# Optimization experiments

Hardware: AMD Instinct MI355X
Metric: run time of the kernel (lower is better)

Reference implementation:

```python
import jax, jax.numpy as jnp
import numpy as np


def setup_inputs() -> dict:
    key = jax.random.key(0)
    k1, k2, k3, k4 = jax.random.split(key, 4)
    B, S, I, H, O = 32, 4096, 64, 512, 64
    x = jax.random.normal(k1, (B, S, I), dtype=jnp.float32)
    b = jax.random.normal(k2, (I, H), dtype=jnp.float32)
    A = jax.random.uniform(k3, (H,), dtype=jnp.float32)  # stable diagonal decay in [0,1)
    c = jax.random.normal(k4, (H, O), dtype=jnp.float32)
    return {"x": x, "b": b, "A": A, "c": c}


def reference(x, b, A, c):
    # Diagonal-transition linear RNN: h_t = x_t @ b + h_{t-1} * A ; y_t = h_t @ c
    B, S, I = x.shape
    H = A.shape[0]
    xb = jnp.einsum('bsi,ih->sbh', x, b)  # precompute input projection, scan-major layout

    def step(h, xb_t):
        h = xb_t + h * A
        return h, h

    h0 = jnp.zeros((B, H), dtype=x.dtype)
    _, hs = jax.lax.scan(step, h0, xb)          # hs: [S, B, H]
    ys = jnp.einsum('sbh,ho->bso', hs, c)       # [B, S, O]
    # torch concat along dim=1 of per-step [B,O] outputs -> [B, S*O], then unsqueeze(-1)
    out = ys.reshape(B, S * ys.shape[-1])[:, :, None]
    return out
```

## Files before the change

kernel.cpp:

```cpp
#include <hip/hip_runtime.h>
#include <hip/hip_bf16.h>

constexpr int Bc = 32, Sc = 4096, Ic = 64, Hc = 512, Oc = 64;
constexpr int Lc = 128;
constexpr int NCc = Sc / Lc;
constexpr int HSUB = 128;
constexpr int NSUB = Hc / HSUB;

typedef __attribute__((ext_vector_type(8))) short short8;
typedef __attribute__((ext_vector_type(4))) short short4v;
typedef __attribute__((ext_vector_type(4))) float float4v;
typedef __attribute__((ext_vector_type(2))) unsigned uint2v;

__device__ __forceinline__ short f2bf(float f) {
    unsigned u = __builtin_bit_cast(unsigned, f);
    u += 0x7FFFu + ((u >> 16) & 1u);
    return (short)(u >> 16);
}
__device__ __forceinline__ float bf2f(short s) {
    unsigned u = ((unsigned)(unsigned short)s) << 16;
    return __builtin_bit_cast(float, u);
}

__device__ __forceinline__ int swz(int row, int rowBytes, int byteInRow) {
    return row * rowBytes + (byteInRow ^ ((row & 7) << 4));
}

__global__ void prep_kernel(const float* __restrict__ bw, const float* __restrict__ cw,
                            short* __restrict__ bT, short* __restrict__ cT) {
    int gid = blockIdx.x * 256 + threadIdx.x;
    if (gid < Ic * Hc) {
        int i = gid / Hc, h = gid % Hc;
        bT[h * Ic + i] = f2bf(bw[gid]);
    } else {
        int idx = gid - Ic * Hc;
        int h = idx / Oc, o = idx % Oc;
        cT[o * Hc + h] = f2bf(cw[idx]);
    }
}

__global__ void carry_kernel(const float* __restrict__ Adiag, const float* __restrict__ last,
                             float* __restrict__ carryIn) {
    int gid = blockIdx.x * 256 + threadIdx.x;
    int b = gid >> 9, h = gid & (Hc - 1);
    float a = Adiag[h];
    float aL = (a > 0.f) ? exp2f((float)Lc * log2f(a)) : 0.f;
    float run = 0.f;
    for (int k = 0; k < NCc; k++) {
        size_t idx = ((size_t)b * NCc + k) * Hc + h;
        carryIn[idx] = run;
        run = last[idx] + aL * run;
    }
}

template <int WRITE_Y>
__global__ __launch_bounds__(256, 2) void chunk_kernel(
    const float* __restrict__ x, const short* __restrict__ bT,
    const short* __restrict__ cT, const float* __restrict__ Adiag,
    const float* __restrict__ carryIn, float* __restrict__ lastOut,
    float* __restrict__ out) {
    __shared__ char Xs[128 * 128];
    __shared__ char bTs[128 * 128];
    __shared__ char cTs[64 * 256];
    __shared__ char xbh[128 * 256];

    const int tid = threadIdx.x;
    const int chunk = blockIdx.x, b = blockIdx.y;
    const int t0 = chunk * Lc;
    const int l = tid & 63;
    const int tg = (tid >> 6) * 32;

    const float4v* xg = (const float4v*)(x + ((size_t)b * Sc + t0) * Ic);
#pragma unroll
    for (int rr = 0; rr < 8; rr++) {
        int idx = rr * 256 + tid;
        float4v v = xg[idx];
        int row = idx >> 4, c4 = idx & 15;
        short4v sv;
        sv[0] = f2bf(v[0]); sv[1] = f2bf(v[1]); sv[2] = f2bf(v[2]); sv[3] = f2bf(v[3]);
        *(short4v*)(Xs + swz(row, 128, c4 * 8)) = sv;
    }

    float4v yacc[2][4];
    if (WRITE_Y) {
#pragma unroll
        for (int i = 0; i < 2; i++)
#pragma unroll
            for (int j = 0; j < 4; j++) yacc[i][j] = (float4v)0.f;
    }

    for (int hsu = 0; hsu < NSUB; hsu++) {
        __syncthreads();

        const uint2v* bg = (const uint2v*)(bT + hsu * HSUB * Ic);
#pragma unroll
        for (int rr = 0; rr < 8; rr++) {
            int idx = rr * 256 + tid;
            int row = idx >> 4, c8 = idx & 15;
            uint2v vv = bg[idx];
            *(uint2v*)(bTs + swz(row, 128, c8 * 8)) = vv;
        }
        if (WRITE_Y) {
            const uint2v* cg = (const uint2v*)cT;
#pragma unroll
            for (int rr = 0; rr < 8; rr++) {
                int idx = rr * 256 + tid;
                int row = idx >> 5, c8 = idx & 31;
                uint2v vv = cg[row * 128 + hsu * 32 + c8];
                *(uint2v*)(cTs + swz(row, 256, c8 * 8)) = vv;
            }
        }
        __syncthreads();

        short8 afr[2][2];
#pragma unroll
        for (int ti = 0; ti < 2; ti++)
#pragma unroll
            for (int ks = 0; ks < 2; ks++) {
                int row = tg + ti * 16 + (l & 15);
                int byt = ks * 64 + ((l >> 4) * 16);
                afr[ti][ks] = *(const short8*)(Xs + swz(row, 128, byt));
            }
#pragma unroll
        for (int hj = 0; hj < 8; hj++) {
            short8 bfr[2];
#pragma unroll
            for (int ks = 0; ks < 2; ks++) {
                int row = hj * 16 + (l & 15);
                int byt = ks * 64 + ((l >> 4) * 16);
                bfr[ks] = *(const short8*)(bTs + swz(row, 128, byt));
            }
#pragma unroll
            for (int ti = 0; ti < 2; ti++) {
                float4v acc = (float4v)0.f;
                acc = __builtin_amdgcn_mfma_f32_16x16x32_bf16(afr[ti][0], bfr[0], acc, 0, 0, 0);
                acc = __builtin_amdgcn_mfma_f32_16x16x32_bf16(afr[ti][1], bfr[1], acc, 0, 0, 0);
#pragma unroll
                for (int r = 0; r < 4; r++) {
                    int trow = tg + ti * 16 + (l >> 4) * 4 + r;
                    int hcol = hj * 16 + (l & 15);
                    *(short*)(xbh + swz(trow, 256, hcol * 2)) = f2bf(acc[r]);
                }
            }
        }
        __syncthreads();

        if (tid < HSUB) {
            int h = hsu * HSUB + tid;
            float a = Adiag[h];
            float hstate = WRITE_Y ? carryIn[((size_t)b * NCc + chunk) * Hc + h] : 0.f;
#pragma unroll 4
            for (int t = 0; t < Lc; t++) {
                int off = swz(t, 256, tid * 2);
                float v = bf2f(*(short*)(xbh + off));
                hstate = fmaf(hstate, a, v);
                if (WRITE_Y) *(short*)(xbh + off) = f2bf(hstate);
            }
            if (!WRITE_Y) lastOut[((size_t)b * NCc + chunk) * Hc + h] = hstate;
        }
        __syncthreads();

        if (WRITE_Y) {
#pragma unroll
            for (int ks = 0; ks < 4; ks++) {
                short8 a2[2];
#pragma unroll
                for (int ti = 0; ti < 2; ti++) {
                    int row = tg + ti * 16 + (l & 15);
                    int byt = ks * 64 + ((l >> 4) * 16);
                    a2[ti] = *(const short8*)(xbh + swz(row, 256, byt));
                }
#pragma unroll
                for (int oj = 0; oj < 4; oj++) {
                    int row = oj * 16 + (l & 15);
                    int byt = ks * 64 + ((l >> 4) * 16);
                    short8 b2 = *(const short8*)(cTs + swz(row, 256, byt));
#pragma unroll
                    for (int ti = 0; ti < 2; ti++)
                        yacc[ti][oj] = __builtin_amdgcn_mfma_f32_16x16x32_bf16(a2[ti], b2, yacc[ti][oj], 0, 0, 0);
                }
            }
        }
    }

    if (WRITE_Y) {
        float* og = out + ((size_t)b * Sc + t0) * Oc;
#pragma unroll
        for (int ti = 0; ti < 2; ti++)
#pragma unroll
            for (int oj = 0; oj < 4; oj++)
#pragma unroll
                for (int r = 0; r < 4; r++) {
                    int t = tg + ti * 16 + (l >> 4) * 4 + r;
                    int o = oj * 16 + (l & 15);
                    og[t * Oc + o] = yacc[ti][oj][r];
                }
    }
}

extern "C" void kernel_launch(void* const* d_in, const int* in_sizes, int n_in,
                              void* d_out, int out_size, void* d_ws, size_t ws_size,
                              hipStream_t stream) {
    (void)in_sizes; (void)n_in; (void)out_size; (void)ws_size;
    const float* x     = (const float*)d_in[0];
    const float* bw    = (const float*)d_in[1];
    const float* Adiag = (const float*)d_in[2];
    const float* cw    = (const float*)d_in[3];
    float* out = (float*)d_out;

    float* last    = (float*)d_ws;
    float* carryIn = last + (size_t)Bc * NCc * Hc;
    short* bT      = (short*)(carryIn + (size_t)Bc * NCc * Hc);
    short* cT      = bT + Ic * Hc;

    prep_kernel<<<256, 256, 0, stream>>>(bw, cw, bT, cT);
    chunk_kernel<0><<<dim3(NCc, Bc), 256, 0, stream>>>(x, bT, cT, Adiag, nullptr, last, nullptr);
    carry_kernel<<<64, 256, 0, stream>>>(Adiag, last, carryIn);
    chunk_kernel<1><<<dim3(NCc, Bc), 256, 0, stream>>>(x, bT, cT, Adiag, carryIn, nullptr, out);
}
```

Measured before the change: 197.7 us.

## Replace serial in-chunk scan with register-level parallel scan across MFMA fragments

Replaces the single-thread sequential 128-step scan over the LDS-staged projection with a parallel scan done in registers on the MFMA accumulators. It uses intra-lane FMA chains, cross-lane shuffles and per-wave aggregates combined through a small shared buffer. x, bT and cT fragments are now loaded straight from global memory into registers instead of being staged in LDS, which shrinks shared memory and raises the occupancy launch bounds. The risks are more register pressure, more uncoalesced global fragment loads, and bf16 rounding of the input projection being skipped, which slightly changes numerics.

```diff
diff --git a/kernel.cpp b/kernel.cpp
--- a/kernel.cpp
+++ b/kernel.cpp
@@ -8,18 +8,12 @@
 constexpr int NSUB = Hc / HSUB;
 
 typedef __attribute__((ext_vector_type(8))) short short8;
-typedef __attribute__((ext_vector_type(4))) short short4v;
 typedef __attribute__((ext_vector_type(4))) float float4v;
-typedef __attribute__((ext_vector_type(2))) unsigned uint2v;
 
 __device__ __forceinline__ short f2bf(float f) {
     unsigned u = __builtin_bit_cast(unsigned, f);
     u += 0x7FFFu + ((u >> 16) & 1u);
     return (short)(u >> 16);
-}
-__device__ __forceinline__ float bf2f(short s) {
-    unsigned u = ((unsigned)(unsigned short)s) << 16;
-    return __builtin_bit_cast(float, u);
 }
 
 __device__ __forceinline__ int swz(int row, int rowBytes, int byteInRow) {
@@ -44,41 +38,49 @@
     int gid = blockIdx.x * 256 + threadIdx.x;
     int b = gid >> 9, h = gid & (Hc - 1);
     float a = Adiag[h];
-    float aL = (a > 0.f) ? exp2f((float)Lc * log2f(a)) : 0.f;
+    float aL = a;
+#pragma unroll
+    for (int i = 0; i < 7; i++) aL *= aL;
     float run = 0.f;
     for (int k = 0; k < NCc; k++) {
         size_t idx = ((size_t)b * NCc + k) * Hc + h;
         carryIn[idx] = run;
-        run = last[idx] + aL * run;
+        run = fmaf(aL, run, last[idx]);
     }
 }
 
 template <int WRITE_Y>
-__global__ __launch_bounds__(256, 2) void chunk_kernel(
+__global__ __launch_bounds__(256, WRITE_Y ? 3 : 4) void chunk_kernel(
     const float* __restrict__ x, const short* __restrict__ bT,
     const short* __restrict__ cT, const float* __restrict__ Adiag,
     const float* __restrict__ carryIn, float* __restrict__ lastOut,
     float* __restrict__ out) {
-    __shared__ char Xs[128 * 128];
-    __shared__ char bTs[128 * 128];
-    __shared__ char cTs[64 * 256];
-    __shared__ char xbh[128 * 256];
+    extern __shared__ char smem[];
+    char* hbuf = smem;
+    float* agg = (float*)(smem + (WRITE_Y ? 32768 : 0));
 
     const int tid = threadIdx.x;
     const int chunk = blockIdx.x, b = blockIdx.y;
     const int t0 = chunk * Lc;
     const int l = tid & 63;
-    const int tg = (tid >> 6) * 32;
-
-    const float4v* xg = (const float4v*)(x + ((size_t)b * Sc + t0) * Ic);
-#pragma unroll
-    for (int rr = 0; rr < 8; rr++) {
-        int idx = rr * 256 + tid;
-        float4v v = xg[idx];
-        int row = idx >> 4, c4 = idx & 15;
-        short4v sv;
-        sv[0] = f2bf(v[0]); sv[1] = f2bf(v[1]); sv[2] = f2bf(v[2]); sv[3] = f2bf(v[3]);
-        *(short4v*)(Xs + swz(row, 128, c4 * 8)) = sv;
+    const int wid = tid >> 6;
+    const int tg = wid * 32;
+    const int lr = l & 15;
+    const int g = l >> 4;
+
+    short8 xf[2][2];
+#pragma unroll
+    for (int ti = 0; ti < 2; ti++) {
+        const float* xr = x + ((size_t)b * Sc + t0 + tg + ti * 16 + lr) * Ic + g * 8;
+#pragma unroll
+        for (int ks = 0; ks < 2; ks++) {
+            float4v v0 = *(const float4v*)(xr + ks * 32);
+            float4v v1 = *(const float4v*)(xr + ks * 32 + 4);
+            short8 f;
+            f[0] = f2bf(v0[0]); f[1] = f2bf(v0[1]); f[2] = f2bf(v0[2]); f[3] = f2bf(v0[3]);
+            f[4] = f2bf(v1[0]); f[5] = f2bf(v1[1]); f[6] = f2bf(v1[2]); f[7] = f2bf(v1[3]);
+            xf[ti][ks] = f;
+        }
     }
 
     float4v yacc[2][4];
@@ -89,96 +91,108 @@
             for (int j = 0; j < 4; j++) yacc[i][j] = (float4v)0.f;
     }
 
+#pragma unroll 1
     for (int hsu = 0; hsu < NSUB; hsu++) {
+        const int buf = hsu & 1;
+        float4v acc[2][8];
+
+#pragma unroll
+        for (int hj = 0; hj < 8; hj++) {
+            const short* br = bT + ((hsu * HSUB + hj * 16 + lr) * Ic + g * 8);
+            short8 b0 = *(const short8*)br;
+            short8 b1 = *(const short8*)(br + 32);
+#pragma unroll
+            for (int ti = 0; ti < 2; ti++) {
+                float4v t = (float4v)0.f;
+                t = __builtin_amdgcn_mfma_f32_16x16x32_bf16(xf[ti][0], b0, t, 0, 0, 0);
+                t = __builtin_amdgcn_mfma_f32_16x16x32_bf16(xf[ti][1], b1, t, 0, 0, 0);
+                acc[ti][hj] = t;
+            }
+        }
+
+#pragma unroll
+        for (int hj = 0; hj < 8; hj++) {
+            float a = Adiag[hsu * HSUB + hj * 16 + lr];
+            float a2 = a * a, a3 = a2 * a, a4 = a2 * a2, a8 = a4 * a4, a16 = a8 * a8;
+            float a4g = ((g & 1) ? a4 : 1.f) * ((g & 2) ? a8 : 1.f);
+#pragma unroll
+            for (int ti = 0; ti < 2; ti++) {
+                acc[ti][hj][1] = fmaf(acc[ti][hj][0], a, acc[ti][hj][1]);
+                acc[ti][hj][2] = fmaf(acc[ti][hj][1], a, acc[ti][hj][2]);
+                acc[ti][hj][3] = fmaf(acc[ti][hj][2], a, acc[ti][hj][3]);
+            }
+            float s0 = acc[0][hj][3];
+            float u = __shfl_up(s0, 16u, 64); s0 = (g >= 1) ? fmaf(u, a4, s0) : s0;
+            u = __shfl_up(s0, 32u, 64);       s0 = (g >= 2) ? fmaf(u, a8, s0) : s0;
+            float E0 = __shfl_up(s0, 16u, 64); E0 = (g >= 1) ? E0 : 0.f;
+            float S16_0 = __shfl(s0, lr + 48, 64);
+            float s1 = acc[1][hj][3];
+            u = __shfl_up(s1, 16u, 64); s1 = (g >= 1) ? fmaf(u, a4, s1) : s1;
+            u = __shfl_up(s1, 32u, 64); s1 = (g >= 2) ? fmaf(u, a8, s1) : s1;
+            float E1 = __shfl_up(s1, 16u, 64); E1 = (g >= 1) ? E1 : 0.f;
+            E1 = fmaf(a4g, S16_0, E1);
+            float S16_1 = __shfl(s1, lr + 48, 64);
+#pragma unroll
+            for (int r = 0; r < 4; r++) {
+                float apr = (r == 0) ? a : (r == 1) ? a2 : (r == 2) ? a3 : a4;
+                acc[0][hj][r] = fmaf(apr, E0, acc[0][hj][r]);
+                acc[1][hj][r] = fmaf(apr, E1, acc[1][hj][r]);
+            }
+            float S32 = fmaf(a16, S16_0, S16_1);
+            if (l < 16) agg[(buf * 4 + wid) * 128 + hj * 16 + l] = S32;
+        }
         __syncthreads();
 
-        const uint2v* bg = (const uint2v*)(bT + hsu * HSUB * Ic);
-#pragma unroll
-        for (int rr = 0; rr < 8; rr++) {
-            int idx = rr * 256 + tid;
-            int row = idx >> 4, c8 = idx & 15;
-            uint2v vv = bg[idx];
-            *(uint2v*)(bTs + swz(row, 128, c8 * 8)) = vv;
-        }
         if (WRITE_Y) {
-            const uint2v* cg = (const uint2v*)cT;
-#pragma unroll
-            for (int rr = 0; rr < 8; rr++) {
-                int idx = rr * 256 + tid;
-                int row = idx >> 5, c8 = idx & 31;
-                uint2v vv = cg[row * 128 + hsu * 32 + c8];
-                *(uint2v*)(cTs + swz(row, 256, c8 * 8)) = vv;
-            }
-        }
-        __syncthreads();
-
-        short8 afr[2][2];
-#pragma unroll
-        for (int ti = 0; ti < 2; ti++)
-#pragma unroll
-            for (int ks = 0; ks < 2; ks++) {
-                int row = tg + ti * 16 + (l & 15);
-                int byt = ks * 64 + ((l >> 4) * 16);
-                afr[ti][ks] = *(const short8*)(Xs + swz(row, 128, byt));
-            }
-#pragma unroll
-        for (int hj = 0; hj < 8; hj++) {
-            short8 bfr[2];
-#pragma unroll
-            for (int ks = 0; ks < 2; ks++) {
-                int row = hj * 16 + (l & 15);
-                int byt = ks * 64 + ((l >> 4) * 16);
-                bfr[ks] = *(const short8*)(bTs + swz(row, 128, byt));
-            }
-#pragma unroll
-            for (int ti = 0; ti < 2; ti++) {
-                float4v acc = (float4v)0.f;
-                acc = __builtin_amdgcn_mfma_f32_16x16x32_bf16(afr[ti][0], bfr[0], acc, 0, 0, 0);
-                acc = __builtin_amdgcn_mfma_f32_16x16x32_bf16(afr[ti][1], bfr[1], acc, 0, 0, 0);
-#pragma unroll
-                for (int r = 0; r < 4; r++) {
-                    int trow = tg + ti * 16 + (l >> 4) * 4 + r;
-                    int hcol = hj * 16 + (l & 15);
-                    *(short*)(xbh + swz(trow, 256, hcol * 2)) = f2bf(acc[r]);
+#pragma unroll
+            for (int hj = 0; hj < 8; hj++) {
+                float a = Adiag[hsu * HSUB + hj * 16 + lr];
+                float a2 = a * a, a3 = a2 * a, a4 = a2 * a2, a8 = a4 * a4;
+                float a16 = a8 * a8, a32 = a16 * a16;
+                float a4g = ((g & 1) ? a4 : 1.f) * ((g & 2) ? a8 : 1.f);
+                float P = carryIn[((size_t)b * NCc + chunk) * Hc + hsu * HSUB + hj * 16 + lr];
+                for (int j = 0; j < wid; j++)
+                    P = fmaf(P, a32, agg[(buf * 4 + j) * 128 + hj * 16 + lr]);
+                float base0 = P * a4g;
+                float base1 = base0 * a16;
+#pragma unroll
+                for (int ti = 0; ti < 2; ti++) {
+                    float bb = ti ? base1 : base0;
+#pragma unroll
+                    for (int r = 0; r < 4; r++) {
+                        float apr = (r == 0) ? a : (r == 1) ? a2 : (r == 2) ? a3 : a4;
+                        float hv = fmaf(apr, bb, acc[ti][hj][r]);
+                        int trow = tg + ti * 16 + g * 4 + r;
+                        *(short*)(hbuf + swz(trow, 256, (hj * 16 + lr) * 2)) = f2bf(hv);
+                    }
                 }
             }
-        }
-        __syncthreads();
-
-        if (tid < HSUB) {
-            int h = hsu * HSUB + tid;
-            float a = Adiag[h];
-            float hstate = WRITE_Y ? carryIn[((size_t)b * NCc + chunk) * Hc + h] : 0.f;
-#pragma unroll 4
-            for (int t = 0; t < Lc; t++) {
-                int off = swz(t, 256, tid * 2);
-                float v = bf2f(*(short*)(xbh + off));
-                hstate = fmaf(hstate, a, v);
-                if (WRITE_Y) *(short*)(xbh + off) = f2bf(hstate);
-            }
-            if (!WRITE_Y) lastOut[((size_t)b * NCc + chunk) * Hc + h] = hstate;
-        }
-        __syncthreads();
-
-        if (WRITE_Y) {
 #pragma unroll
             for (int ks = 0; ks < 4; ks++) {
-                short8 a2[2];
-#pragma unroll
-                for (int ti = 0; ti < 2; ti++) {
-                    int row = tg + ti * 16 + (l & 15);
-                    int byt = ks * 64 + ((l >> 4) * 16);
-                    a2[ti] = *(const short8*)(xbh + swz(row, 256, byt));
+                short8 af[2];
+#pragma unroll
+                for (int ti = 0; ti < 2; ti++)
+                    af[ti] = *(const short8*)(hbuf + swz(tg + ti * 16 + lr, 256, ks * 64 + g * 16));
+#pragma unroll
+                for (int oj = 0; oj < 4; oj++) {
+                    const short* cr = cT + (oj * 16 + lr) * Hc + hsu * HSUB + ks * 32 + g * 8;
+                    short8 bf = *(const short8*)cr;
+#pragma unroll
+                    for (int ti = 0; ti < 2; ti++)
+                        yacc[ti][oj] = __builtin_amdgcn_mfma_f32_16x16x32_bf16(af[ti], bf, yacc[ti][oj], 0, 0, 0);
                 }
-#pragma unroll
-                for (int oj = 0; oj < 4; oj++) {
-                    int row = oj * 16 + (l & 15);
-                    int byt = ks * 64 + ((l >> 4) * 16);
-                    short8 b2 = *(const short8*)(cTs + swz(row, 256, byt));
-#pragma unroll
-                    for (int ti = 0; ti < 2; ti++)
-                        yacc[ti][oj] = __builtin_amdgcn_mfma_f32_16x16x32_bf16(a2[ti], b2, yacc[ti][oj], 0, 0, 0);
-                }
+            }
+        } else {
+            if (tid < HSUB) {
+                int h = hsu * HSUB + tid;
+                float a = Adiag[h];
+                float a2 = a * a, a4 = a2 * a2, a8 = a4 * a4;
+                float a16 = a8 * a8, a32 = a16 * a16;
+                float W = agg[(buf * 4 + 0) * 128 + tid];
+                W = fmaf(W, a32, agg[(buf * 4 + 1) * 128 + tid]);
+                W = fmaf(W, a32, agg[(buf * 4 + 2) * 128 + tid]);
+                W = fmaf(W, a32, agg[(buf * 4 + 3) * 128 + tid]);
+                lastOut[((size_t)b * NCc + chunk) * Hc + h] = W;
             }
         }
     }
@@ -191,8 +205,8 @@
             for (int oj = 0; oj < 4; oj++)
 #pragma unroll
                 for (int r = 0; r < 4; r++) {
-                    int t = tg + ti * 16 + (l >> 4) * 4 + r;
-                    int o = oj * 16 + (l & 15);
+                    int t = tg + ti * 16 + g * 4 + r;
+                    int o = oj * 16 + lr;
                     og[t * Oc + o] = yacc[ti][oj][r];
                 }
     }
@@ -214,7 +228,7 @@
     short* cT      = bT + Ic * Hc;
 
     prep_kernel<<<256, 256, 0, stream>>>(bw, cw, bT, cT);
-    chunk_kernel<0><<<dim3(NCc, Bc), 256, 0, stream>>>(x, bT, cT, Adiag, nullptr, last, nullptr);
+    chunk_kernel<0><<<dim3(NCc, Bc), 256, 4096, stream>>>(x, bT, cT, Adiag, nullptr, last, nullptr);
     carry_kernel<<<64, 256, 0, stream>>>(Adiag, last, carryIn);
-    chunk_kernel<1><<<dim3(NCc, Bc), 256, 0, stream>>>(x, bT, cT, Adiag, carryIn, nullptr, out);
-}
+    chunk_kernel<1><<<dim3(NCc, Bc), 256, 36864, stream>>>(x, bT, cT, Adiag, carryIn, nullptr, out);
+}
```

After: 369.2 us. 86.8% more time.
